# Optimization experiments

Measured on AMD Instinct MI355X. Metric: run time of the kernel, lower is better.

The kernel has to match this reference:

```python
import jax, jax.numpy as jnp
import numpy as np

B, L, H, E = 8, 1024, 8, 64
HIST = 512


def setup_inputs() -> dict:
    key = jax.random.key(0)
    ks = jax.random.split(key, 6)
    shp = (B, L, H, E)
    q, k, v, qd, kd, vd = (jax.random.normal(kk, shp, dtype=jnp.float32) for kk in ks)
    # DoubleTriangularCausalMask surrogate: strictly-upper-triangular causal mask (diagonal=1)
    attn_mask = jnp.triu(jnp.ones((L, L), dtype=bool), k=1)[None, None]  # (1,1,L,S)
    return {
        "queries": q, "keys": k, "values": v,
        "queries_drawn": qd, "keys_drawn": kd, "values_drawn": vd,
        "attn_mask": attn_mask, "history_len": HIST,
    }


def reference(queries, keys, values, queries_drawn, keys_drawn, values_drawn, attn_mask, history_len):
    # drawn_y=True branch of FullFixedTimeCausalConstructiveAttention with history_len set.
    B, L, H, E = queries.shape
    scale = 1.0 / float(np.sqrt(E))
    hist = history_len
    idx = jnp.arange(hist, L)

    # queries[:, hist:] = queries_drawn[:, hist:]
    q_eff = jnp.concatenate([queries[:, :hist], queries_drawn[:, hist:]], axis=1)

    scores = jnp.einsum('blhe,bshe->bhls', q_eff, keys)  # (B,H,L,S)
    # diagonal positions l>=hist use drawn keys: q_eff[l] . keys_drawn[l]
    diag_scores = jnp.einsum('blhe,blhe->bhl', q_eff[:, hist:], keys_drawn[:, hist:])
    scores = scores.at[:, :, idx, idx].set(diag_scores)

    scores = jnp.where(attn_mask, -jnp.inf, scores)
    A = jax.nn.softmax(scale * scores, axis=-1)  # (B,H,L,S); dropout rate 0 in eval

    # values substitution on the diagonal (l==s, l>=hist) is a rank-1 correction;
    # avoids materializing the torch (B,H,D,L,S) repeated tensor.
    V = jnp.einsum('bhls,bshd->blhd', A, values)
    diag_A = A[:, :, idx, idx]                      # (B,H,L-hist)
    delta = values_drawn[:, hist:] - values[:, hist:]  # (B,L-hist,H,D)
    V = V.at[:, hist:].add(jnp.transpose(diag_A, (0, 2, 1))[..., None] * delta)
    return V
```

## Files before the change

kernel.cpp:

```cpp
#include <hip/hip_runtime.h>

#define BB   8
#define LL   1024
#define HH   8
#define EE   64
#define HIST 512
#define KSTR 72

typedef _Float16 f16;
typedef _Float16 v8h __attribute__((ext_vector_type(8)));
typedef float    v4f __attribute__((ext_vector_type(4)));

__device__ __forceinline__ void load16f(const float* __restrict__ p, float* __restrict__ f) {
  const float4* p4 = reinterpret_cast<const float4*>(p);
  float4 a = p4[0], b = p4[1], c = p4[2], d = p4[3];
  f[0]=a.x;  f[1]=a.y;  f[2]=a.z;  f[3]=a.w;
  f[4]=b.x;  f[5]=b.y;  f[6]=b.z;  f[7]=b.w;
  f[8]=c.x;  f[9]=c.y;  f[10]=c.z; f[11]=c.w;
  f[12]=d.x; f[13]=d.y; f[14]=d.z; f[15]=d.w;
}

struct TileState {
  v4f   o[4];
  float m[4], l[4], pd[4];
};

__device__ __forceinline__ void tile_update(
    TileState& st, const v8h* __restrict__ qf, bool dt, bool drawn,
    const f16* __restrict__ Ks, const f16* __restrict__ Vt,
    f16* __restrict__ Psw, const float* __restrict__ zd,
    int w, int ln, int lq)
{
  v4f S[4];
#pragma unroll
  for (int nb = 0; nb < 4; ++nb) {
    const f16* krow = &Ks[(nb * 16 + ln) * KSTR + 8 * lq];
    v8h b0 = *reinterpret_cast<const v8h*>(krow);
    v8h b1 = *reinterpret_cast<const v8h*>(krow + 32);
    v4f acc = (v4f){0.f, 0.f, 0.f, 0.f};
    acc = __builtin_amdgcn_mfma_f32_16x16x32_f16(qf[0], b0, acc, 0, 0, 0);
    acc = __builtin_amdgcn_mfma_f32_16x16x32_f16(qf[1], b1, acc, 0, 0, 0);
    S[nb] = acc;
  }

  float z[4][4];
#pragma unroll
  for (int nb = 0; nb < 4; ++nb)
#pragma unroll
    for (int r = 0; r < 4; ++r) z[nb][r] = S[nb][r] * 0.125f;

  if (dt) {
#pragma unroll
    for (int nb = 0; nb < 4; ++nb) {
      const int col = nb * 16 + ln;
#pragma unroll
      for (int r = 0; r < 4; ++r) {
        const int rowt = w * 16 + lq * 4 + r;
        if (col > rowt)                 z[nb][r] = -1e30f;
        else if (drawn && col == rowt)  z[nb][r] = zd[rowt];
      }
    }
  }

  float mx[4];
#pragma unroll
  for (int r = 0; r < 4; ++r)
    mx[r] = fmaxf(fmaxf(z[0][r], z[1][r]), fmaxf(z[2][r], z[3][r]));
#pragma unroll
  for (int s = 1; s < 16; s <<= 1)
#pragma unroll
    for (int r = 0; r < 4; ++r) mx[r] = fmaxf(mx[r], __shfl_xor(mx[r], s));

  float al[4];
#pragma unroll
  for (int r = 0; r < 4; ++r) {
    const float mn = fmaxf(st.m[r], mx[r]);
    al[r] = __expf(st.m[r] - mn);
    st.m[r] = mn;
  }

  float p[4][4], rsum[4] = {0.f, 0.f, 0.f, 0.f}, pdl[4] = {0.f, 0.f, 0.f, 0.f};
#pragma unroll
  for (int nb = 0; nb < 4; ++nb) {
    const int col = nb * 16 + ln;
#pragma unroll
    for (int r = 0; r < 4; ++r) {
      const float pv = __expf(z[nb][r] - st.m[r]);
      p[nb][r] = pv;
      rsum[r] += pv;
      if (dt && drawn && col == (w * 16 + lq * 4 + r)) pdl[r] = pv;
    }
  }
#pragma unroll
  for (int s = 1; s < 16; s <<= 1)
#pragma unroll
    for (int r = 0; r < 4; ++r) rsum[r] += __shfl_xor(rsum[r], s);
  if (dt && drawn) {
#pragma unroll
    for (int s = 1; s < 16; s <<= 1)
#pragma unroll
      for (int r = 0; r < 4; ++r) pdl[r] += __shfl_xor(pdl[r], s);
#pragma unroll
    for (int r = 0; r < 4; ++r) st.pd[r] = pdl[r];
  }
#pragma unroll
  for (int r = 0; r < 4; ++r) st.l[r] = st.l[r] * al[r] + rsum[r];
#pragma unroll
  for (int nb = 0; nb < 4; ++nb)
#pragma unroll
    for (int r = 0; r < 4; ++r) st.o[nb][r] *= al[r];

#pragma unroll
  for (int nb = 0; nb < 4; ++nb)
#pragma unroll
    for (int r = 0; r < 4; ++r)
      Psw[(lq * 4 + r) * KSTR + nb * 16 + ln] = (f16)p[nb][r];
  v8h pA0 = *reinterpret_cast<const v8h*>(&Psw[ln * KSTR + 8 * lq]);
  v8h pA1 = *reinterpret_cast<const v8h*>(&Psw[ln * KSTR + 32 + 8 * lq]);

#pragma unroll
  for (int nb = 0; nb < 4; ++nb) {
    const f16* vrow = &Vt[(nb * 16 + ln) * KSTR + 8 * lq];
    v8h v0 = *reinterpret_cast<const v8h*>(vrow);
    v8h v1 = *reinterpret_cast<const v8h*>(vrow + 32);
    st.o[nb] = __builtin_amdgcn_mfma_f32_16x16x32_f16(pA0, v0, st.o[nb], 0, 0, 0);
    st.o[nb] = __builtin_amdgcn_mfma_f32_16x16x32_f16(pA1, v1, st.o[nb], 0, 0, 0);
  }
}

extern "C" __global__ __launch_bounds__(256)
void ftcca_pair(const float* __restrict__ Q,  const float* __restrict__ K,
                const float* __restrict__ V,  const float* __restrict__ Qd,
                const float* __restrict__ Kd, const float* __restrict__ Vd,
                float* __restrict__ out)
{
  __shared__ f16   Ks[64 * KSTR];
  __shared__ f16   Vt[64 * KSTR];
  __shared__ f16   Ps[4][16 * KSTR];
  __shared__ float zdiag[64];

  const int bh  = blockIdx.x & 63;
  const int a   = blockIdx.x >> 6;
  const int qtA = 15 - a;
  const int qtB = a;
  const int b   = bh >> 3, h = bh & 7;
  const int t   = threadIdx.x;
  const int w    = t >> 6;
  const int lane = t & 63;
  const int ln   = lane & 15;
  const int lq   = lane >> 4;
  const int rs   = t >> 2;
  const int es0  = (t & 3) * 16;

  const size_t base = ((size_t)b * LL * HH + h) * EE;
  const int ROWF = HH * EE;

  {
    const int l = qtA * 64 + rs;
    const float* qrow = Qd + base + (size_t)l * ROWF + es0;
    const float* krow = Kd + base + (size_t)l * ROWF + es0;
    float par = 0.f;
#pragma unroll
    for (int i = 0; i < 16; ++i) par += qrow[i] * krow[i];
    par += __shfl_xor(par, 1);
    par += __shfl_xor(par, 2);
    if ((t & 3) == 0) zdiag[rs] = 0.125f * par;
  }

  const int rowt_q = w * 16 + ln;
  v8h qfA[2], qfB[2];
  {
    const float* pa = Qd + base + (size_t)(qtA * 64 + rowt_q) * ROWF;
    const float* pb = Q  + base + (size_t)(qtB * 64 + rowt_q) * ROWF;
#pragma unroll
    for (int c = 0; c < 2; ++c) {
      const float* xa = pa + 32 * c + 8 * lq;
      const float* xb = pb + 32 * c + 8 * lq;
#pragma unroll
      for (int j = 0; j < 8; ++j) { qfA[c][j] = (f16)xa[j]; qfB[c][j] = (f16)xb[j]; }
    }
  }

  TileState stA, stB;
#pragma unroll
  for (int nb = 0; nb < 4; ++nb) { stA.o[nb] = (v4f){0,0,0,0}; stB.o[nb] = (v4f){0,0,0,0}; }
#pragma unroll
  for (int r = 0; r < 4; ++r) {
    stA.m[r] = -1e30f; stA.l[r] = 0.f; stA.pd[r] = 0.f;
    stB.m[r] = -1e30f; stB.l[r] = 0.f; stB.pd[r] = 0.f;
  }

  float tk[16], tv[16];
  load16f(K + base + (size_t)rs * ROWF + es0, tk);
  load16f(V + base + (size_t)rs * ROWF + es0, tv);

  for (int i = 0; i <= qtA; ++i) {
    __syncthreads();
    {
      v8h k0, k1;
#pragma unroll
      for (int j = 0; j < 8; ++j) { k0[j] = (f16)tk[j]; k1[j] = (f16)tk[8 + j]; }
      v8h* kd0 = reinterpret_cast<v8h*>(&Ks[rs * KSTR + es0]);
      kd0[0] = k0;
      kd0[1] = k1;
#pragma unroll
      for (int jj = 0; jj < 16; ++jj) Vt[(es0 + jj) * KSTR + rs] = (f16)tv[jj];
    }
    __syncthreads();

    if (i < qtA) {
      const size_t goff = base + (size_t)((i + 1) * 64 + rs) * ROWF + es0;
      load16f(K + goff, tk);
      load16f(V + goff, tv);
    }

    tile_update(stA, qfA, i == qtA, true,  Ks, Vt, Ps[w], zdiag, w, ln, lq);
    if (i <= qtB)
      tile_update(stB, qfB, i == qtB, false, Ks, Vt, Ps[w], zdiag, w, ln, lq);
  }

  float invA[4], invB[4];
#pragma unroll
  for (int r = 0; r < 4; ++r) { invA[r] = 1.f / stA.l[r]; invB[r] = 1.f / stB.l[r]; }

#pragma unroll
  for (int nb = 0; nb < 4; ++nb) {
    const int col = nb * 16 + ln;
#pragma unroll
    for (int r = 0; r < 4; ++r) {
      {
        const int l = qtA * 64 + w * 16 + lq * 4 + r;
        const size_t g = base + (size_t)l * ROWF + col;
        float val = stA.o[nb][r] * invA[r];
        val += (stA.pd[r] * invA[r]) * (Vd[g] - V[g]);
        out[g] = val;
      }
      {
        const int l = qtB * 64 + w * 16 + lq * 4 + r;
        const size_t g = base + (size_t)l * ROWF + col;
        out[g] = stB.o[nb][r] * invB[r];
      }
    }
  }
}

extern "C" void kernel_launch(void* const* d_in, const int* in_sizes, int n_in,
                              void* d_out, int out_size, void* d_ws, size_t ws_size,
                              hipStream_t stream) {
  const float* q  = (const float*)d_in[0];
  const float* k  = (const float*)d_in[1];
  const float* v  = (const float*)d_in[2];
  const float* qd = (const float*)d_in[3];
  const float* kd = (const float*)d_in[4];
  const float* vd = (const float*)d_in[5];
  float* out = (float*)d_out;

  ftcca_pair<<<dim3(512), dim3(256), 0, stream>>>(q, k, v, qd, kd, vd, out);
}
```

Baseline: 162.8 us.

## Split paired query tiles into separate blocks, swizzle V transpose, use exp2

```diff
diff --git a/kernel.cpp b/kernel.cpp
--- a/kernel.cpp
+++ b/kernel.cpp
@@ -7,9 +7,20 @@
 #define HIST 512
 #define KSTR 72
 
+#define SCALE2 0.18033688011112043f
+
 typedef _Float16 f16;
-typedef _Float16 v8h __attribute__((ext_vector_type(8)));
-typedef float    v4f __attribute__((ext_vector_type(4)));
+typedef _Float16 v8h   __attribute__((ext_vector_type(8)));
+typedef _Float16 f16x2 __attribute__((ext_vector_type(2)));
+typedef float    v4f   __attribute__((ext_vector_type(4)));
+
+__device__ __forceinline__ float fexp2(float x) {
+#if __has_builtin(__builtin_amdgcn_exp2f)
+  return __builtin_amdgcn_exp2f(x);
+#else
+  return __expf(x * 0.6931471805599453f);
+#endif
+}
 
 __device__ __forceinline__ void load16f(const float* __restrict__ p, float* __restrict__ f) {
   const float4* p4 = reinterpret_cast<const float4*>(p);
@@ -20,6 +31,13 @@
   f[12]=d.x; f[13]=d.y; f[14]=d.z; f[15]=d.w;
 }
 
+__device__ __forceinline__ void load8f(const float* __restrict__ p, float* __restrict__ f) {
+  const float4* p4 = reinterpret_cast<const float4*>(p);
+  float4 a = p4[0], b = p4[1];
+  f[0]=a.x; f[1]=a.y; f[2]=a.z; f[3]=a.w;
+  f[4]=b.x; f[5]=b.y; f[6]=b.z; f[7]=b.w;
+}
+
 struct TileState {
   v4f   o[4];
   float m[4], l[4], pd[4];
@@ -47,7 +65,7 @@
 #pragma unroll
   for (int nb = 0; nb < 4; ++nb)
 #pragma unroll
-    for (int r = 0; r < 4; ++r) z[nb][r] = S[nb][r] * 0.125f;
+    for (int r = 0; r < 4; ++r) z[nb][r] = S[nb][r] * SCALE2;
 
   if (dt) {
 #pragma unroll
@@ -75,7 +93,7 @@
 #pragma unroll
   for (int r = 0; r < 4; ++r) {
     const float mn = fmaxf(st.m[r], mx[r]);
-    al[r] = __expf(st.m[r] - mn);
+    al[r] = fexp2(st.m[r] - mn);
     st.m[r] = mn;
   }
 
@@ -85,7 +103,7 @@
     const int col = nb * 16 + ln;
 #pragma unroll
     for (int r = 0; r < 4; ++r) {
-      const float pv = __expf(z[nb][r] - st.m[r]);
+      const float pv = fexp2(z[nb][r] - st.m[r]);
       p[nb][r] = pv;
       rsum[r] += pv;
       if (dt && drawn && col == (w * 16 + lq * 4 + r)) pdl[r] = pv;
@@ -120,19 +138,21 @@
 
 #pragma unroll
   for (int nb = 0; nb < 4; ++nb) {
-    const f16* vrow = &Vt[(nb * 16 + ln) * KSTR + 8 * lq];
-    v8h v0 = *reinterpret_cast<const v8h*>(vrow);
-    v8h v1 = *reinterpret_cast<const v8h*>(vrow + 32);
+    const int d   = nb * 16 + ln;
+    const int dsw = (d >> 3) & 7;
+    const f16* vbase = &Vt[d * KSTR];
+    v8h v0 = *reinterpret_cast<const v8h*>(vbase + (((lq    ) ^ dsw) & 7) * 8);
+    v8h v1 = *reinterpret_cast<const v8h*>(vbase + (((lq + 4) ^ dsw) & 7) * 8);
     st.o[nb] = __builtin_amdgcn_mfma_f32_16x16x32_f16(pA0, v0, st.o[nb], 0, 0, 0);
     st.o[nb] = __builtin_amdgcn_mfma_f32_16x16x32_f16(pA1, v1, st.o[nb], 0, 0, 0);
   }
 }
 
-extern "C" __global__ __launch_bounds__(256)
-void ftcca_pair(const float* __restrict__ Q,  const float* __restrict__ K,
-                const float* __restrict__ V,  const float* __restrict__ Qd,
-                const float* __restrict__ Kd, const float* __restrict__ Vd,
-                float* __restrict__ out)
+extern "C" __global__ __launch_bounds__(256, 4)
+void ftcca_split(const float* __restrict__ Q,  const float* __restrict__ K,
+                 const float* __restrict__ V,  const float* __restrict__ Qd,
+                 const float* __restrict__ Kd, const float* __restrict__ Vd,
+                 float* __restrict__ out)
 {
   __shared__ f16   Ks[64 * KSTR];
   __shared__ f16   Vt[64 * KSTR];
@@ -141,8 +161,8 @@
 
   const int bh  = blockIdx.x & 63;
   const int a   = blockIdx.x >> 6;
-  const int qtA = 15 - a;
-  const int qtB = a;
+  const int qt  = 15 - a;
+  const bool drawn = (qt >= 8);
   const int b   = bh >> 3, h = bh & 7;
   const int t   = threadIdx.x;
   const int w    = t >> 6;
@@ -151,12 +171,14 @@
   const int lq   = lane >> 4;
   const int rs   = t >> 2;
   const int es0  = (t & 3) * 16;
+  const int vr0  = (t >> 3) * 2;
+  const int vd0  = (t & 7) * 8;
 
   const size_t base = ((size_t)b * LL * HH + h) * EE;
   const int ROWF = HH * EE;
 
-  {
-    const int l = qtA * 64 + rs;
+  if (drawn) {
+    const int l = qt * 64 + rs;
     const float* qrow = Qd + base + (size_t)l * ROWF + es0;
     const float* krow = Kd + base + (size_t)l * ROWF + es0;
     float par = 0.f;
@@ -164,37 +186,34 @@
     for (int i = 0; i < 16; ++i) par += qrow[i] * krow[i];
     par += __shfl_xor(par, 1);
     par += __shfl_xor(par, 2);
-    if ((t & 3) == 0) zdiag[rs] = 0.125f * par;
+    if ((t & 3) == 0) zdiag[rs] = SCALE2 * par;
   }
 
   const int rowt_q = w * 16 + ln;
-  v8h qfA[2], qfB[2];
+  const float* qsrc = drawn ? Qd : Q;
+  v8h qf[2];
   {
-    const float* pa = Qd + base + (size_t)(qtA * 64 + rowt_q) * ROWF;
-    const float* pb = Q  + base + (size_t)(qtB * 64 + rowt_q) * ROWF;
+    const float* pq = qsrc + base + (size_t)(qt * 64 + rowt_q) * ROWF;
 #pragma unroll
     for (int c = 0; c < 2; ++c) {
-      const float* xa = pa + 32 * c + 8 * lq;
-      const float* xb = pb + 32 * c + 8 * lq;
-#pragma unroll
-      for (int j = 0; j < 8; ++j) { qfA[c][j] = (f16)xa[j]; qfB[c][j] = (f16)xb[j]; }
-    }
-  }
-
-  TileState stA, stB;
-#pragma unroll
-  for (int nb = 0; nb < 4; ++nb) { stA.o[nb] = (v4f){0,0,0,0}; stB.o[nb] = (v4f){0,0,0,0}; }
-#pragma unroll
-  for (int r = 0; r < 4; ++r) {
-    stA.m[r] = -1e30f; stA.l[r] = 0.f; stA.pd[r] = 0.f;
-    stB.m[r] = -1e30f; stB.l[r] = 0.f; stB.pd[r] = 0.f;
-  }
+      const float* x = pq + 32 * c + 8 * lq;
+#pragma unroll
+      for (int j = 0; j < 8; ++j) qf[c][j] = (f16)x[j];
+    }
+  }
+
+  TileState st;
+#pragma unroll
+  for (int nb = 0; nb < 4; ++nb) st.o[nb] = (v4f){0, 0, 0, 0};
+#pragma unroll
+  for (int r = 0; r < 4; ++r) { st.m[r] = -1e30f; st.l[r] = 0.f; st.pd[r] = 0.f; }
 
   float tk[16], tv[16];
   load16f(K + base + (size_t)rs * ROWF + es0, tk);
-  load16f(V + base + (size_t)rs * ROWF + es0, tv);
-
-  for (int i = 0; i <= qtA; ++i) {
+  load8f(V + base + (size_t)vr0 * ROWF + vd0, tv);
+  load8f(V + base + (size_t)(vr0 + 1) * ROWF + vd0, tv + 8);
+
+  for (int i = 0; i <= qt; ++i) {
     __syncthreads();
     {
       v8h k0, k1;
@@ -203,43 +222,41 @@
       v8h* kd0 = reinterpret_cast<v8h*>(&Ks[rs * KSTR + es0]);
       kd0[0] = k0;
       kd0[1] = k1;
-#pragma unroll
-      for (int jj = 0; jj < 16; ++jj) Vt[(es0 + jj) * KSTR + rs] = (f16)tv[jj];
+      const int vswz = vr0 >> 3;
+#pragma unroll
+      for (int dd = 0; dd < 8; ++dd) {
+        const int d  = vd0 + dd;
+        const int ch = (vswz ^ (d >> 3)) & 7;
+        f16x2 val; val[0] = (f16)tv[dd]; val[1] = (f16)tv[8 + dd];
+        *reinterpret_cast<f16x2*>(&Vt[d * KSTR + ch * 8 + (vr0 & 7)]) = val;
+      }
     }
     __syncthreads();
 
-    if (i < qtA) {
-      const size_t goff = base + (size_t)((i + 1) * 64 + rs) * ROWF + es0;
-      load16f(K + goff, tk);
-      load16f(V + goff, tv);
-    }
-
-    tile_update(stA, qfA, i == qtA, true,  Ks, Vt, Ps[w], zdiag, w, ln, lq);
-    if (i <= qtB)
-      tile_update(stB, qfB, i == qtB, false, Ks, Vt, Ps[w], zdiag, w, ln, lq);
-  }
-
-  float invA[4], invB[4];
-#pragma unroll
-  for (int r = 0; r < 4; ++r) { invA[r] = 1.f / stA.l[r]; invB[r] = 1.f / stB.l[r]; }
+    if (i < qt) {
+      const size_t r0 = (size_t)((i + 1) * 64);
+      load16f(K + base + (r0 + rs) * ROWF + es0, tk);
+      load8f(V + base + (r0 + vr0) * ROWF + vd0, tv);
+      load8f(V + base + (r0 + vr0 + 1) * ROWF + vd0, tv + 8);
+    }
+
+    tile_update(st, qf, i == qt, drawn, Ks, Vt, Ps[w], zdiag, w, ln, lq);
+  }
+
+  float inv[4];
+#pragma unroll
+  for (int r = 0; r < 4; ++r) inv[r] = 1.f / st.l[r];
 
 #pragma unroll
   for (int nb = 0; nb < 4; ++nb) {
     const int col = nb * 16 + ln;
 #pragma unroll
     for (int r = 0; r < 4; ++r) {
-      {
-        const int l = qtA * 64 + w * 16 + lq * 4 + r;
-        const size_t g = base + (size_t)l * ROWF + col;
-        float val = stA.o[nb][r] * invA[r];
-        val += (stA.pd[r] * invA[r]) * (Vd[g] - V[g]);
-        out[g] = val;
-      }
-      {
-        const int l = qtB * 64 + w * 16 + lq * 4 + r;
-        const size_t g = base + (size_t)l * ROWF + col;
-        out[g] = stB.o[nb][r] * invB[r];
-      }
+      const int l = qt * 64 + w * 16 + lq * 4 + r;
+      const size_t g = base + (size_t)l * ROWF + col;
+      float val = st.o[nb][r] * inv[r];
+      if (drawn) val += (st.pd[r] * inv[r]) * (Vd[g] - V[g]);
+      out[g] = val;
     }
   }
 }
@@ -255,5 +272,5 @@
   const float* vd = (const float*)d_in[5];
   float* out = (float*)d_out;
 
-  ftcca_pair<<<dim3(512), dim3(256), 0, stream>>>(q, k, v, qd, kd, vd, out);
-}
+  ftcca_split<<<dim3(1024), dim3(256), 0, stream>>>(q, k, v, qd, kd, vd, out);
+}
```

Measured after the change: 164.5 us. About the same (+1.0%).
